# Kernel tuning notes

Hardware: AMD Instinct MI355X
Metric: run time of the kernel (lower is better)

## Reference

```python
import jax, jax.numpy as jnp
import numpy as np

D = 384; QK = 48; E = 768; LOCAL = E - D
NB = 8; NTOK = 100; NEG = -1e30
B = 128; S = 100; NPTS = 256


def layernorm(x, w, eps=1e-5):
    mu = jnp.mean(x, axis=-1, keepdims=True)
    var = jnp.mean((x - mu) ** 2, axis=-1, keepdims=True)
    return (x - mu) * jax.lax.rsqrt(var + eps) * w


def attend(q, k, v, bias=None):
    scale = 1.0 / jnp.sqrt(jnp.asarray(q.shape[-1], q.dtype))
    s = jnp.einsum('bqd,bkd->bqk', q, k) * scale
    if bias is not None:
        s = s + bias
    return jnp.einsum('bqk,bkd->bqd', jax.nn.softmax(s, axis=-1), v)


def setup_inputs() -> dict:
    key = jax.random.key(0)
    ks = jax.random.split(key, 16)
    s_exp = 0.5 / (D ** 0.5) / 2.0   # 0.5 / sqrt(residual_depth) / expand_factor
    s_prj = 1.0 / (D ** 0.5) / 2.0 / NB
    return {
        'q': jax.random.randint(ks[0], (B, S), 0, NTOK),
        'pts': jax.random.randint(ks[1], (B, NPTS, 2), 0, NTOK),
        'emb': jax.random.normal(ks[2], (NTOK, D), jnp.float32),
        'pt_emb': jax.random.normal(ks[3], (NTOK, D // 2), jnp.float32),
        'norm_w': jnp.ones((D,), jnp.float32),
        'out_w': jax.random.normal(ks[4], (NTOK, D), jnp.float32) / (D ** 0.5),
        'ln1': jnp.ones((NB, D), jnp.float32),
        'expand': s_exp * jax.random.normal(ks[5], (NB, 2 * QK + 2 * E, D), jnp.float32),
        'project1': s_prj * jax.random.normal(ks[6], (NB, D, E), jnp.float32),
        'bias_mult': jnp.ones((NB,), jnp.float32),
        'ln2': jnp.ones((NB, D), jnp.float32),
        'Wq': s_exp * jax.random.normal(ks[7], (NB, QK + 2 * LOCAL, D), jnp.float32),
        'Wkv': s_exp * jax.random.normal(ks[8], (NB, QK + 2 * D, D), jnp.float32),
        'project2': s_prj * jax.random.normal(ks[9], (NB, D, E), jnp.float32),
    }


def _forward(q, pts, emb, pt_emb, norm_w, out_w, ln1, expand, project1, bias_mult, ln2, Wq, Wkv, project2):
    x = emb[q]                                        # [B,S,D]
    kv = pt_emb[pts].reshape(pts.shape[0], -1, D)     # [B,NPTS,D] (pairs of 2D coords fold into D)
    x = layernorm(x, norm_w)

    pos = jnp.arange(x.shape[1])
    pbb = (pos[None, :] - pos[:, None]).astype(x.dtype)  # position bias base (j - i)
    allowed = pos[None, :] <= pos[:, None]                # causal: attend to past + self

    def step(h, p):
        w_ln1, W_e, W_p1, bm, w_ln2, W_q, W_kv, W_p2 = p
        # --- latent self-attention block ---
        bias = jnp.where(allowed, jax.nn.softplus(bm) * pbb, NEG)
        n = layernorm(h, w_ln1)
        proj = n @ W_e.T                                  # [B,S,2*QK+2*E]
        qr = proj[..., :QK]
        kr = proj[..., QK:2 * QK]
        lin = proj[..., 2 * QK:2 * QK + E]
        pre = proj[..., 2 * QK + E:]
        geglu = lin * jax.nn.gelu(pre, approximate=False)
        attn = attend(qr, kr, geglu[..., LOCAL:], bias)
        h = h + jnp.concatenate([geglu[..., :LOCAL], attn], axis=-1) @ W_p1.T
        # --- latent cross-attention block ---
        n = layernorm(h, w_ln2)
        pq = n @ W_q.T                                    # [B,S,QK+2*LOCAL]
        qr2 = pq[..., :QK]
        g_local = pq[..., QK:QK + LOCAL] * jax.nn.gelu(pq[..., QK + LOCAL:], approximate=False)
        pk = kv @ W_kv.T                                  # [B,NPTS,QK+2*D]
        k2 = pk[..., :QK]
        g_val = pk[..., QK:QK + D] * jax.nn.gelu(pk[..., QK + D:], approximate=False)
        attn2 = attend(qr2, k2, g_val)
        h = h + jnp.concatenate([g_local, attn2], axis=-1) @ W_p2.T
        return h, None

    x, _ = jax.lax.scan(step, x, (ln1, expand, project1, bias_mult, ln2, Wq, Wkv, project2))
    x = layernorm(x, norm_w)
    return x @ out_w.T                                    # [B,S,NTOK]


def reference(q, pts, emb, pt_emb, norm_w, out_w, ln1, expand, project1, bias_mult, ln2, Wq, Wkv, project2):
    return _forward(q, pts, emb, pt_emb, norm_w, out_w, ln1, expand, project1, bias_mult, ln2, Wq, Wkv, project2)
```

## Files before the change

### kernel.cpp

```cpp
#include <hip/hip_runtime.h>
#include <hip/hip_bf16.h>
#include <math.h>

#define B_    128
#define S_    100
#define D_    384
#define QK_   48
#define E_    768
#define LOCAL_ 384
#define NB_   8
#define NTOK_ 100
#define NPTS_ 256
#define M_    (B_*S_)

typedef unsigned short ushort;
typedef __attribute__((ext_vector_type(8))) short  bf16x8;
typedef __attribute__((ext_vector_type(8))) unsigned short ushort8v;
typedef __attribute__((ext_vector_type(4))) float  f32x4;

#define MFMA(a,b,c) __builtin_amdgcn_mfma_f32_16x16x32_bf16(a,b,c,0,0,0)

static __device__ __forceinline__ float gelu_f(float x) {
    float y = 1.5957691216057308f * (x + 0.044715f * x * x * x);
    float e = __expf(y);
    float t = 1.0f - 2.0f / (e + 1.0f);
    return 0.5f * x * (1.0f + t);
}
static __device__ __forceinline__ ushort f2b(float f) {
    union { float f; unsigned u; } x; x.f = f;
    unsigned r = x.u + 0x7FFFu + ((x.u >> 16) & 1u);
    return (ushort)(r >> 16);
}
static __device__ __forceinline__ float b2f(ushort u) {
    union { unsigned u; float f; } x; x.u = ((unsigned)u) << 16;
    return x.f;
}

__global__ __launch_bounds__(256)
void ln_rows(const float* __restrict__ X, const float* __restrict__ w,
             ushort* __restrict__ Y, int nrows)
{
    int row = blockIdx.x * 4 + (threadIdx.x >> 6);
    if (row >= nrows) return;
    int lane = threadIdx.x & 63;
    const float* x = X + (size_t)row * D_;
    float v[6]; float s = 0.f;
    #pragma unroll
    for (int t = 0; t < 6; ++t) { v[t] = x[lane + 64*t]; s += v[t]; }
    #pragma unroll
    for (int off = 32; off; off >>= 1) s += __shfl_xor(s, off);
    float mu = s * (1.f/(float)D_);
    float q = 0.f;
    #pragma unroll
    for (int t = 0; t < 6; ++t) { float d = v[t]-mu; q += d*d; }
    #pragma unroll
    for (int off = 32; off; off >>= 1) q += __shfl_xor(q, off);
    float rs = rsqrtf(q * (1.f/(float)D_) + 1e-5f);
    #pragma unroll
    for (int t = 0; t < 6; ++t)
        Y[(size_t)row*D_ + lane + 64*t] = f2b((v[t]-mu)*rs*w[lane + 64*t]);
}

__global__ __launch_bounds__(256)
void x_init(const int* __restrict__ qtok, const float* __restrict__ emb,
            const float* __restrict__ w, float* __restrict__ Y, int nrows)
{
    int row = blockIdx.x * 4 + (threadIdx.x >> 6);
    if (row >= nrows) return;
    int lane = threadIdx.x & 63;
    const float* x = emb + (size_t)qtok[row] * D_;
    float v[6]; float s = 0.f;
    #pragma unroll
    for (int t = 0; t < 6; ++t) { v[t] = x[lane + 64*t]; s += v[t]; }
    #pragma unroll
    for (int off = 32; off; off >>= 1) s += __shfl_xor(s, off);
    float mu = s * (1.f/(float)D_);
    float q = 0.f;
    #pragma unroll
    for (int t = 0; t < 6; ++t) { float d = v[t]-mu; q += d*d; }
    #pragma unroll
    for (int off = 32; off; off >>= 1) q += __shfl_xor(q, off);
    float rs = rsqrtf(q * (1.f/(float)D_) + 1e-5f);
    float* y = Y + (size_t)row * D_;
    #pragma unroll
    for (int t = 0; t < 6; ++t) y[lane + 64*t] = (v[t]-mu)*rs*w[lane + 64*t];
}

#define WE_SZ  (1632*384)
#define P1_SZ  (384*768)
#define WQ_SZ  (816*384)
#define P2_SZ  (384*768)
#define WTOT   (WE_SZ + P1_SZ + WQ_SZ + P2_SZ)

static __device__ __forceinline__ void wsplit(float v, ushort* wh, ushort* wl, size_t o) {
    ushort h = f2b(v);
    wh[o] = h; wl[o] = f2b(v - b2f(h));
}

__global__ __launch_bounds__(256)
void wconv_all_hi(const float* __restrict__ expand, const float* __restrict__ proj1,
                  const float* __restrict__ wq, const float* __restrict__ proj2,
                  ushort* __restrict__ wh)
{
    int i = blockIdx.x*256 + threadIdx.x;
    if (i >= WTOT) return;
    int blk = blockIdx.y;
    float v;
    if (i < WE_SZ) v = expand[(size_t)blk*WE_SZ + i];
    else if (i < WE_SZ+P1_SZ) v = proj1[(size_t)blk*P1_SZ + (i - WE_SZ)];
    else if (i < WE_SZ+P1_SZ+WQ_SZ) v = wq[(size_t)blk*WQ_SZ + (i - WE_SZ - P1_SZ)];
    else v = proj2[(size_t)blk*P2_SZ + (i - WE_SZ - P1_SZ - WQ_SZ)];
    wh[(size_t)blk*WTOT + i] = f2b(v);
}

__global__ __launch_bounds__(256)
void wconv_hi(const float* __restrict__ we, const float* __restrict__ p1,
              const float* __restrict__ wq, const float* __restrict__ p2,
              ushort* __restrict__ wh)
{
    int i = blockIdx.x*256 + threadIdx.x;
    if (i >= WTOT) return;
    float v;
    if (i < WE_SZ) v = we[i];
    else if (i < WE_SZ+P1_SZ) v = p1[i - WE_SZ];
    else if (i < WE_SZ+P1_SZ+WQ_SZ) v = wq[i - WE_SZ - P1_SZ];
    else v = p2[i - WE_SZ - P1_SZ - WQ_SZ];
    wh[i] = f2b(v);
}

__global__ __launch_bounds__(256)
void wconv1(const float* __restrict__ src, int n,
            ushort* __restrict__ wh, ushort* __restrict__ wl)
{
    int i = blockIdx.x*256 + threadIdx.x;
    if (i >= n) return;
    wsplit(src[i], wh, wl, i);
}

__global__ __launch_bounds__(256)
void pconv(const float* __restrict__ src, ushort* __restrict__ dst)
{
    int i = blockIdx.x*256 + threadIdx.x;
    if (i >= 128*192) return;
    int r = i / 192;
    dst[i] = (r < NTOK_) ? f2b(src[i]) : 0;
}

__global__ __launch_bounds__(256)
void mm_bt64(const ushort* __restrict__ A1, int lda1, int K1,
             const ushort* __restrict__ A2, int lda2,
             const ushort* __restrict__ Wgh, const ushort* __restrict__ Wgl,
             float* __restrict__ C, int ldc, int N, int K, int accum)
{
    __shared__ ushort Ah[64][72], Wh[64][72], Wl[64][72];
    int tid = threadIdx.x;
    int row0 = blockIdx.y*64, col0 = blockIdx.x*64;
    int srow = tid >> 3;
    int sseg = (tid & 7) * 8;
    int wid = tid >> 6, lane = tid & 63;
    int wr = wid >> 1, wc = wid & 1;
    int fr = lane & 15, fg = lane >> 4;
    f32x4 acc[2][2] = {};
    for (int k0 = 0; k0 < K; k0 += 64) {
        ushort8v va[2], vc[2], vd[2];
        #pragma unroll
        for (int p = 0; p < 2; ++p) {
            int r = p*32 + srow;
            int arow = row0 + r;
            int wrow = col0 + r;
            int gk = k0 + sseg;
            if (gk < K1) va[p] = *(const ushort8v*)(A1 + (size_t)arow*lda1 + gk);
            else         va[p] = *(const ushort8v*)(A2 + (size_t)arow*lda2 + (gk-K1));
            if (wrow >= N) wrow = N - 1;
            vc[p] = *(const ushort8v*)(Wgh + (size_t)wrow*K + gk);
            vd[p] = *(const ushort8v*)(Wgl + (size_t)wrow*K + gk);
        }
        __syncthreads();
        #pragma unroll
        for (int p = 0; p < 2; ++p) {
            int r = p*32 + srow;
            *(ushort8v*)&Ah[r][sseg] = va[p];
            *(ushort8v*)&Wh[r][sseg] = vc[p];
            *(ushort8v*)&Wl[r][sseg] = vd[p];
        }
        __syncthreads();
        #pragma unroll
        for (int kk = 0; kk < 64; kk += 32) {
            bf16x8 a[2], b_h[2], b_l[2];
            #pragma unroll
            for (int s = 0; s < 2; ++s) {
                a[s]   = *(const bf16x8*)&Ah[wr*32 + s*16 + fr][kk + fg*8];
                b_h[s] = *(const bf16x8*)&Wh[wc*32 + s*16 + fr][kk + fg*8];
                b_l[s] = *(const bf16x8*)&Wl[wc*32 + s*16 + fr][kk + fg*8];
            }
            #pragma unroll
            for (int s = 0; s < 2; ++s)
                #pragma unroll
                for (int u = 0; u < 2; ++u)
                    acc[s][u] = MFMA(a[s], b_h[u], acc[s][u]);
            #pragma unroll
            for (int s = 0; s < 2; ++s)
                #pragma unroll
                for (int u = 0; u < 2; ++u)
                    acc[s][u] = MFMA(a[s], b_l[u], acc[s][u]);
        }
        __syncthreads();
    }
    #pragma unroll
    for (int s = 0; s < 2; ++s) {
        int r = row0 + wr*32 + s*16 + fg*4;
        #pragma unroll
        for (int u = 0; u < 2; ++u) {
            int c = col0 + wc*32 + u*16 + fr;
            if (c < N) {
                #pragma unroll
                for (int j = 0; j < 4; ++j) {
                    size_t o = (size_t)(r+j)*ldc + c;
                    C[o] = accum ? (C[o] + acc[s][u][j]) : acc[s][u][j];
                }
            }
        }
    }
}

__global__ __launch_bounds__(256)
void mm_bt2(const ushort* __restrict__ A1, int lda1, int K1,
            const ushort* __restrict__ A2, int lda2,
            const ushort* __restrict__ Wgh,
            float* __restrict__ C, int ldc, int N, int K, int accum)
{
    __shared__ ushort As[128*32], Whs[64*32];
    int tid = threadIdx.x;
    int lane = tid & 63, wid = tid >> 6;
    int row0 = blockIdx.y*128, col0 = blockIdx.x*64;
    int wr = wid >> 1, wc = wid & 1;
    int fr = lane & 15, fg = lane >> 4;
    int gsl = (fg ^ ((fr >> 1) & 3)) * 8;
    int sr = tid >> 2, sg0 = tid & 3;
    int g = sg0 ^ ((sr >> 1) & 3);
    int wrow = col0 + sr; if (wrow >= N) wrow = N - 1;

    ushort8v va[2], vh;
    auto loadk = [&](int k0) {
        const ushort* Asrc; int lda, kk;
        if (k0 < K1) { Asrc = A1; lda = lda1; kk = k0; }
        else         { Asrc = A2; lda = lda2; kk = k0 - K1; }
        #pragma unroll
        for (int i = 0; i < 2; ++i)
            va[i] = *(const ushort8v*)(Asrc + (size_t)(row0 + sr + i*64)*lda + kk + g*8);
        vh = *(const ushort8v*)(Wgh + (size_t)wrow*K + k0 + g*8);
    };

    f32x4 acc[4][2] = {};
    loadk(0);
    for (int k0 = 0; k0 < K; k0 += 32) {
        __syncthreads();
        #pragma unroll
        for (int i = 0; i < 2; ++i)
            *(ushort8v*)&As[(sr + i*64)*32 + sg0*8] = va[i];
        *(ushort8v*)&Whs[sr*32 + sg0*8] = vh;
        if (k0 + 32 < K) loadk(k0 + 32);
        __syncthreads();
        bf16x8 a[4], bh[2];
        #pragma unroll
        for (int s = 0; s < 4; ++s) {
            int r = wr*64 + s*16 + fr;
            a[s] = *(const bf16x8*)&As[r*32 + gsl];
        }
        #pragma unroll
        for (int u = 0; u < 2; ++u) {
            int r = wc*32 + u*16 + fr;
            bh[u] = *(const bf16x8*)&Whs[r*32 + gsl];
        }
        #pragma unroll
        for (int s = 0; s < 4; ++s)
            #pragma unroll
            for (int u = 0; u < 2; ++u)
                acc[s][u] = MFMA(a[s], bh[u], acc[s][u]);
    }
    #pragma unroll
    for (int s = 0; s < 4; ++s) {
        int rb = row0 + wr*64 + s*16 + fg*4;
        #pragma unroll
        for (int u = 0; u < 2; ++u) {
            int c = col0 + wc*32 + u*16 + fr;
            if (c < N) {
                #pragma unroll
                for (int j = 0; j < 4; ++j) {
                    size_t o = (size_t)(rb+j)*ldc + c;
                    C[o] = accum ? (C[o] + acc[s][u][j]) : acc[s][u][j];
                }
            }
        }
    }
}

__global__ __launch_bounds__(256)
void mm_fused2(const ushort* __restrict__ Ag, int lda,
               const ushort* __restrict__ Wqh,
               int Nq, int nqt, float* __restrict__ Qout, int ldq,
               const ushort* __restrict__ W1h, const ushort* __restrict__ W2h,
               ushort* __restrict__ Oh, int ldo, int K)
{
    __shared__ ushort As[128*32];
    __shared__ ushort Xs[2][64*32];
    int tid = threadIdx.x;
    int lane = tid & 63, wid = tid >> 6;
    int row0 = blockIdx.y*128;
    int wr = wid >> 1, wc = wid & 1;
    int fr = lane & 15, fg = lane >> 4;
    int gsl = (fg ^ ((fr >> 1) & 3)) * 8;
    int sr = tid >> 2, sg0 = tid & 3;
    int g = sg0 ^ ((sr >> 1) & 3);

    if ((int)blockIdx.x < nqt) {
        int col0 = blockIdx.x*64;
        int wrow = col0 + sr; if (wrow >= Nq) wrow = Nq - 1;
        ushort8v va[2], vh;
        auto loadk = [&](int k0) {
            #pragma unroll
            for (int i = 0; i < 2; ++i)
                va[i] = *(const ushort8v*)(Ag + (size_t)(row0 + sr + i*64)*lda + k0 + g*8);
            vh = *(const ushort8v*)(Wqh + (size_t)wrow*K + k0 + g*8);
        };
        f32x4 acc[4][2] = {};
        loadk(0);
        for (int k0 = 0; k0 < K; k0 += 32) {
            __syncthreads();
            #pragma unroll
            for (int i = 0; i < 2; ++i)
                *(ushort8v*)&As[(sr + i*64)*32 + sg0*8] = va[i];
            *(ushort8v*)&Xs[0][sr*32 + sg0*8] = vh;
            if (k0 + 32 < K) loadk(k0 + 32);
            __syncthreads();
            bf16x8 a[4], bh[2];
            #pragma unroll
            for (int s = 0; s < 4; ++s) {
                int r = wr*64 + s*16 + fr;
                a[s] = *(const bf16x8*)&As[r*32 + gsl];
            }
            #pragma unroll
            for (int u = 0; u < 2; ++u) {
                int r = wc*32 + u*16 + fr;
                bh[u] = *(const bf16x8*)&Xs[0][r*32 + gsl];
            }
            #pragma unroll
            for (int s = 0; s < 4; ++s)
                #pragma unroll
                for (int u = 0; u < 2; ++u)
                    acc[s][u] = MFMA(a[s], bh[u], acc[s][u]);
        }
        #pragma unroll
        for (int s = 0; s < 4; ++s) {
            int rb = row0 + wr*64 + s*16 + fg*4;
            #pragma unroll
            for (int u = 0; u < 2; ++u) {
                int c = col0 + wc*32 + u*16 + fr;
                if (c < Nq) {
                    #pragma unroll
                    for (int j = 0; j < 4; ++j)
                        Qout[(size_t)(rb+j)*ldq + c] = acc[s][u][j];
                }
            }
        }
    } else {
        int col0 = ((int)blockIdx.x - nqt)*64;
        ushort8v va[2], vw0, vw2;
        auto loadk = [&](int k0) {
            #pragma unroll
            for (int i = 0; i < 2; ++i)
                va[i] = *(const ushort8v*)(Ag + (size_t)(row0 + sr + i*64)*lda + k0 + g*8);
            size_t wro = (size_t)(col0 + sr)*K + k0 + g*8;
            vw0 = *(const ushort8v*)(W1h + wro);
            vw2 = *(const ushort8v*)(W2h + wro);
        };
        f32x4 acc1[4][2] = {}, acc2[4][2] = {};
        loadk(0);
        for (int k0 = 0; k0 < K; k0 += 32) {
            __syncthreads();
            #pragma unroll
            for (int i = 0; i < 2; ++i)
                *(ushort8v*)&As[(sr + i*64)*32 + sg0*8] = va[i];
            {
                int o = sr*32 + sg0*8;
                *(ushort8v*)&Xs[0][o] = vw0;
                *(ushort8v*)&Xs[1][o] = vw2;
            }
            if (k0 + 32 < K) loadk(k0 + 32);
            __syncthreads();
            bf16x8 a[4], b1[2], b2[2];
            #pragma unroll
            for (int s = 0; s < 4; ++s) {
                int r = wr*64 + s*16 + fr;
                a[s] = *(const bf16x8*)&As[r*32 + gsl];
            }
            #pragma unroll
            for (int u = 0; u < 2; ++u) {
                int r = wc*32 + u*16 + fr;
                b1[u] = *(const bf16x8*)&Xs[0][r*32 + gsl];
                b2[u] = *(const bf16x8*)&Xs[1][r*32 + gsl];
            }
            #pragma unroll
            for (int s = 0; s < 4; ++s)
                #pragma unroll
                for (int u = 0; u < 2; ++u) {
                    acc1[s][u] = MFMA(a[s], b1[u], acc1[s][u]);
                    acc2[s][u] = MFMA(a[s], b2[u], acc2[s][u]);
                }
        }
        #pragma unroll
        for (int s = 0; s < 4; ++s) {
            int rb = row0 + wr*64 + s*16 + fg*4;
            #pragma unroll
            for (int u = 0; u < 2; ++u) {
                int c = col0 + wc*32 + u*16 + fr;
                #pragma unroll
                for (int j = 0; j < 4; ++j) {
                    float gg = acc1[s][u][j] * gelu_f(acc2[s][u][j]);
                    Oh[(size_t)(rb+j)*ldo + c] = f2b(gg);
                }
            }
        }
    }
}

__global__ __launch_bounds__(256)
void pk_mm(const ushort* __restrict__ A,
           const ushort* __restrict__ Wh_, const ushort* __restrict__ Wl_,
           float* __restrict__ P12)
{
    __shared__ ushort Ah[64][72], Wh[64][72], Wl[64][72];
    int tid = threadIdx.x;
    int z = blockIdx.z, blk = z >> 1, half = z & 1;
    int row0 = blockIdx.y*64, col0 = blockIdx.x*64;
    int srow = tid >> 3, sseg = (tid & 7) * 8;
    int wid = tid >> 6, lane = tid & 63;
    int wr = wid >> 1, wc = wid & 1;
    int fr = lane & 15, fg = lane >> 4;
    const ushort* Wbh = Wh_ + (size_t)blk*816*384 + half*192;
    const ushort* Wbl = Wl_ + (size_t)blk*816*384 + half*192;
    float* C = P12 + (size_t)z*128*816;
    f32x4 acc[2][2] = {};
    for (int k0 = 0; k0 < 192; k0 += 64) {
        ushort8v va[2], vc[2], vd[2];
        #pragma unroll
        for (int p = 0; p < 2; ++p) {
            int r = p*32 + srow;
            int wrow = col0 + r; if (wrow >= 816) wrow = 815;
            int gk = k0 + sseg;
            va[p] = *(const ushort8v*)(A + (size_t)(row0 + r)*192 + gk);
            vc[p] = *(const ushort8v*)(Wbh + (size_t)wrow*384 + gk);
            vd[p] = *(const ushort8v*)(Wbl + (size_t)wrow*384 + gk);
        }
        __syncthreads();
        #pragma unroll
        for (int p = 0; p < 2; ++p) {
            int r = p*32 + srow;
            *(ushort8v*)&Ah[r][sseg] = va[p];
            *(ushort8v*)&Wh[r][sseg] = vc[p];
            *(ushort8v*)&Wl[r][sseg] = vd[p];
        }
        __syncthreads();
        #pragma unroll
        for (int kk = 0; kk < 64; kk += 32) {
            bf16x8 a[2], b_h[2], b_l[2];
            #pragma unroll
            for (int s = 0; s < 2; ++s) {
                a[s]   = *(const bf16x8*)&Ah[wr*32 + s*16 + fr][kk + fg*8];
                b_h[s] = *(const bf16x8*)&Wh[wc*32 + s*16 + fr][kk + fg*8];
                b_l[s] = *(const bf16x8*)&Wl[wc*32 + s*16 + fr][kk + fg*8];
            }
            #pragma unroll
            for (int s = 0; s < 2; ++s)
                #pragma unroll
                for (int u = 0; u < 2; ++u)
                    acc[s][u] = MFMA(a[s], b_h[u], acc[s][u]);
            #pragma unroll
            for (int s = 0; s < 2; ++s)
                #pragma unroll
                for (int u = 0; u < 2; ++u)
                    acc[s][u] = MFMA(a[s], b_l[u], acc[s][u]);
        }
        __syncthreads();
    }
    #pragma unroll
    for (int s = 0; s < 2; ++s) {
        int r = row0 + wr*32 + s*16 + fg*4;
        #pragma unroll
        for (int u = 0; u < 2; ++u) {
            int c = col0 + wc*32 + u*16 + fr;
            if (c < 816) {
                #pragma unroll
                for (int j = 0; j < 4; ++j)
                    C[(size_t)(r+j)*816 + c] = acc[s][u][j];
            }
        }
    }
}

__global__ __launch_bounds__(256)
void pv2(const ushort* __restrict__ P, int ldp, long sP,
         const ushort* __restrict__ V, int ldv, long sV,
         ushort* __restrict__ Oh, int ldo, long sO,
         int Mrows, int K, int Kv)
{
    __shared__ ushort Ps[64][40];
    __shared__ ushort Vs[128*32];
    const ushort* Pb = P + (size_t)blockIdx.z * sP;
    const ushort* Vb = V + (size_t)blockIdx.z * sV;
    ushort* Ohb = Oh + (size_t)blockIdx.z * sO;
    int tid = threadIdx.x;
    int row0 = blockIdx.y*64, col0 = blockIdx.x*128;
    int wid = tid >> 6, lane = tid & 63;
    int fr = lane & 15, fg = lane >> 4;
    int prow = tid >> 2, pseg = (tid & 3) * 8;
    int vk = tid & 31, vcb = (tid >> 5) * 8;

    ushort8v pv_, vv[2];
    auto loadk = [&](int k0) {
        pv_ = (ushort8v){0,0,0,0,0,0,0,0};
        int grow = row0 + prow;
        if (grow < Mrows)
            pv_ = *(const ushort8v*)(Pb + (size_t)grow*ldp + k0 + pseg);
        vv[0] = (ushort8v){0,0,0,0,0,0,0,0};
        vv[1] = (ushort8v){0,0,0,0,0,0,0,0};
        int gk = k0 + vk;
        if (gk < Kv) {
            #pragma unroll
            for (int i = 0; i < 2; ++i)
                vv[i] = *(const ushort8v*)(Vb + (size_t)gk*ldv + col0 + vcb + i*64);
        }
    };

    f32x4 acc[4][2] = {};
    loadk(0);
    for (int k0 = 0; k0 < K; k0 += 32) {
        __syncthreads();
        *(ushort8v*)&Ps[prow][pseg] = pv_;
        #pragma unroll
        for (int i = 0; i < 2; ++i) {
            #pragma unroll
            for (int e = 0; e < 8; ++e) {
                int c = vcb + i*64 + e;
                Vs[c*32 + (vk & 7) + 8*((vk >> 3) ^ ((c >> 3) & 3))] = vv[i][e];
            }
        }
        if (k0 + 32 < K) loadk(k0 + 32);
        __syncthreads();
        bf16x8 a[4], b[2];
        #pragma unroll
        for (int s = 0; s < 4; ++s)
            a[s] = *(const bf16x8*)&Ps[s*16 + fr][fg*8];
        #pragma unroll
        for (int u = 0; u < 2; ++u) {
            int c = wid*32 + u*16 + fr;
            b[u] = *(const bf16x8*)&Vs[c*32 + 8*(fg ^ ((c >> 3) & 3))];
        }
        #pragma unroll
        for (int s = 0; s < 4; ++s)
            #pragma unroll
            for (int u = 0; u < 2; ++u)
                acc[s][u] = MFMA(a[s], b[u], acc[s][u]);
    }
    #pragma unroll
    for (int s = 0; s < 4; ++s) {
        int rbase = row0 + s*16 + fg*4;
        #pragma unroll
        for (int u = 0; u < 2; ++u) {
            int c = col0 + wid*32 + u*16 + fr;
            #pragma unroll
            for (int j = 0; j < 4; ++j) {
                int r = rbase + j;
                if (r < Mrows)
                    Ohb[(size_t)r*ldo + c] = f2b(acc[s][u][j]);
            }
        }
    }
}

__global__ __launch_bounds__(256)
void attn1_score(const float* __restrict__ qk, const float* __restrict__ bm, int blk,
                 ushort* __restrict__ P)
{
    __shared__ float qrs[50][QK_];
    __shared__ float krs[S_][QK_+1];
    int b = blockIdx.x, r0 = blockIdx.y*50;
    int tid = threadIdx.x;
    for (int idx = tid; idx < 50*QK_; idx += 256) {
        int r = idx / QK_, c = idx % QK_;
        qrs[r][c] = qk[((size_t)(b*S_ + r0 + r))*96 + c];
    }
    for (int idx = tid; idx < S_*QK_; idx += 256) {
        int r = idx / QK_, c = idx % QK_;
        krs[r][c] = qk[((size_t)(b*S_ + r))*96 + 48 + c];
    }
    __syncthreads();
    float bmv = bm[blk];
    float sp = (bmv > 20.f) ? bmv : log1pf(expf(bmv));
    const float scale = 0.14433756729740643f;
    int w = tid >> 6, lane = tid & 63;
    for (int t = 0; t < 13; ++t) {
        int li = w + 4*t;
        if (li >= 50) break;
        int i = r0 + li;
        int j1 = lane, j2 = lane + 64;
        float s1 = -1e30f, s2 = -1e30f;
        if (j1 <= i) {
            float acc = 0.f;
            #pragma unroll
            for (int l = 0; l < QK_; ++l) acc += qrs[li][l]*krs[j1][l];
            s1 = acc*scale + sp*(float)(j1 - i);
        }
        if (j2 <= i) {
            float acc = 0.f;
            #pragma unroll
            for (int l = 0; l < QK_; ++l) acc += qrs[li][l]*krs[j2][l];
            s2 = acc*scale + sp*(float)(j2 - i);
        }
        float m = fmaxf(s1, s2);
        #pragma unroll
        for (int off = 32; off; off >>= 1) m = fmaxf(m, __shfl_xor(m, off));
        float p1 = (j1 <= i) ? expf(s1 - m) : 0.f;
        float p2 = (j2 <= i) ? expf(s2 - m) : 0.f;
        float sum = p1 + p2;
        #pragma unroll
        for (int off = 32; off; off >>= 1) sum += __shfl_xor(sum, off);
        float inv = 1.f / sum;
        ushort* prow = P + ((size_t)(b*S_) + i)*128;
        prow[j1] = f2b(p1*inv);
        prow[j2] = f2b(p2*inv);
    }
}

__global__ __launch_bounds__(256)
void attn2_score(const float* __restrict__ q2, const float* __restrict__ k2,
                 ushort* __restrict__ P)
{
    __shared__ float ks[NPTS_][QK_+1];
    int b = blockIdx.x, r0 = blockIdx.y*20;
    int tid = threadIdx.x;
    for (int idx = tid; idx < NPTS_*QK_; idx += 256) {
        int r = idx / QK_, c = idx % QK_;
        ks[r][c] = k2[((size_t)(b*NPTS_ + r))*QK_ + c];
    }
    __syncthreads();
    const float scale = 0.14433756729740643f;
    int w = tid >> 6, lane = tid & 63;
    for (int t = 0; t < 5; ++t) {
        int i = r0 + w + 4*t;
        const float* qr = q2 + ((size_t)(b*S_ + i))*QK_;
        float s[4] = {0.f,0.f,0.f,0.f};
        for (int l = 0; l < QK_; ++l) {
            float ql = qr[l];
            #pragma unroll
            for (int r = 0; r < 4; ++r) s[r] += ql * ks[lane + 64*r][l];
        }
        #pragma unroll
        for (int r = 0; r < 4; ++r) s[r] *= scale;
        float m = fmaxf(fmaxf(s[0],s[1]), fmaxf(s[2],s[3]));
        #pragma unroll
        for (int off = 32; off; off >>= 1) m = fmaxf(m, __shfl_xor(m, off));
        float p[4]; float sum = 0.f;
        #pragma unroll
        for (int r = 0; r < 4; ++r) { p[r] = expf(s[r]-m); sum += p[r]; }
        #pragma unroll
        for (int off = 32; off; off >>= 1) sum += __shfl_xor(sum, off);
        float inv = 1.f / sum;
        ushort* prow = P + ((size_t)(b*S_) + i)*256;
        #pragma unroll
        for (int r = 0; r < 4; ++r) prow[lane + 64*r] = f2b(p[r]*inv);
    }
}

__global__ __launch_bounds__(256)
void pk_gather(const int* __restrict__ pts, const float* __restrict__ P12, int blk,
               float* __restrict__ k2, ushort* __restrict__ gv)
{
    int pair = blockIdx.x*4 + (threadIdx.x >> 6);
    int lane = threadIdx.x & 63;
    const float* P1 = P12 + (size_t)(blk*2 + 0)*128*816;
    const float* P2 = P12 + (size_t)(blk*2 + 1)*128*816;
    int t0 = pts[2*pair], t1 = pts[2*pair+1];
    const float* a = P1 + (size_t)t0*816;
    const float* c = P2 + (size_t)t1*816;
    if (lane < QK_) k2[(size_t)pair*QK_ + lane] = a[lane] + c[lane];
    #pragma unroll
    for (int t = 0; t < 6; ++t) {
        int i = lane + 64*t;
        float lin = a[48 + i] + c[48 + i];
        float pre = a[432 + i] + c[432 + i];
        gv[(size_t)pair*D_ + i] = f2b(lin * gelu_f(pre));
    }
}

extern "C" void kernel_launch(void* const* d_in, const int* in_sizes, int n_in,
                              void* d_out, int out_size, void* d_ws, size_t ws_size,
                              hipStream_t stream)
{
    const int*   qtok  = (const int*)d_in[0];
    const int*   pts   = (const int*)d_in[1];
    const float* emb   = (const float*)d_in[2];
    const float* ptemb = (const float*)d_in[3];
    const float* normw = (const float*)d_in[4];
    const float* outw  = (const float*)d_in[5];
    const float* ln1   = (const float*)d_in[6];
    const float* expand= (const float*)d_in[7];
    const float* proj1 = (const float*)d_in[8];
    const float* bm    = (const float*)d_in[9];
    const float* ln2   = (const float*)d_in[10];
    const float* Wq    = (const float*)d_in[11];
    const float* Wkv   = (const float*)d_in[12];
    const float* proj2 = (const float*)d_in[13];
    float* out = (float*)d_out;

    char* base = (char*)d_ws;
    size_t off = 0;
    auto alloc = [&](size_t bytes){ void* p = base + off; off += (bytes + 255) & ~(size_t)255; return p; };
    float*  h     = (float*) alloc((size_t)M_*D_*4);
    ushort* nh    = (ushort*)alloc((size_t)M_*D_*2);
    float*  qk1   = (float*) alloc((size_t)M_*96*4);
    ushort* gegl  = (ushort*)alloc((size_t)M_*E_*2);
    ushort* atb   = (ushort*)alloc((size_t)M_*D_*2);
    ushort* Pbuf  = (ushort*)alloc((size_t)M_*256*2);
    ushort* gv    = (ushort*)alloc((size_t)B_*NPTS_*D_*2);
    float*  P12   = (float*) alloc((size_t)16*128*816*4);
    float*  k2    = (float*) alloc((size_t)B_*NPTS_*QK_*4);
    ushort* wkvh  = (ushort*)alloc((size_t)NB_*816*384*2);
    ushort* wkvl  = (ushort*)alloc((size_t)NB_*816*384*2);
    ushort* ptp   = (ushort*)alloc((size_t)128*192*2);
    ushort* obh   = (ushort*)alloc((size_t)NTOK_*D_*2);
    ushort* obl   = (ushort*)alloc((size_t)NTOK_*D_*2);

    size_t rem = (ws_size > off) ? (ws_size - off) : 0;
    bool fits8 = rem >= ((size_t)NB_ * WTOT * 2 + 1024);
    int nlay = fits8 ? NB_ : 1;
    ushort* wbh = (ushort*)alloc((size_t)nlay*WTOT*2);
    size_t wstride = fits8 ? (size_t)WTOT : 0;

    float*  qr2   = qk1;
    ushort* gloc  = gegl;

    const size_t oWE = 0;
    const size_t oP1 = WE_SZ;
    const size_t oWQ = WE_SZ + P1_SZ;
    const size_t oP2 = WE_SZ + P1_SZ + WQ_SZ;

    x_init<<<M_/4, 256, 0, stream>>>(qtok, emb, normw, h, M_);
    pconv<<<(128*192 + 255)/256, 256, 0, stream>>>(ptemb, ptp);
    wconv1<<<(NB_*816*384 + 255)/256, 256, 0, stream>>>(Wkv, NB_*816*384, wkvh, wkvl);
    pk_mm<<<dim3(13, 2, 16), 256, 0, stream>>>(ptp, wkvh, wkvl, P12);
    if (fits8)
        wconv_all_hi<<<dim3((WTOT+255)/256, NB_), 256, 0, stream>>>(
            expand, proj1, Wq, proj2, wbh);

    for (int blk = 0; blk < NB_; ++blk) {
        if (!fits8)
            wconv_hi<<<(WTOT+255)/256, 256, 0, stream>>>(
                expand + (size_t)blk*WE_SZ, proj1 + (size_t)blk*P1_SZ,
                Wq + (size_t)blk*WQ_SZ, proj2 + (size_t)blk*P2_SZ, wbh);
        const ushort* Lh = wbh + wstride*blk;

        ln_rows<<<M_/4, 256, 0, stream>>>(h, ln1 + blk*D_, nh, M_);
        mm_fused2<<<dim3(14, M_/128), 256, 0, stream>>>(nh, D_,
            Lh + oWE, 96, 2, qk1, 96,
            Lh + oWE + (size_t)96*D_, Lh + oWE + (size_t)864*D_,
            gegl, E_, D_);
        attn1_score<<<dim3(B_,2), 256, 0, stream>>>(qk1, bm, blk, Pbuf);
        pv2<<<dim3(3,2,B_), 256, 0, stream>>>(Pbuf, 128, (long)S_*128,
            gegl + LOCAL_, E_, (long)S_*E_,
            atb, D_, (long)S_*D_, S_, 128, S_);
        mm_bt2<<<dim3(6, M_/128), 256, 0, stream>>>(gegl, E_, D_, atb, D_,
            Lh + oP1, h, D_, D_, E_, 1);

        ln_rows<<<M_/4, 256, 0, stream>>>(h, ln2 + blk*D_, nh, M_);
        mm_fused2<<<dim3(7, M_/128), 256, 0, stream>>>(nh, D_,
            Lh + oWQ, 48, 1, qr2, 48,
            Lh + oWQ + (size_t)48*D_, Lh + oWQ + (size_t)432*D_,
            gloc, D_, D_);
        pk_gather<<<B_*NPTS_/4, 256, 0, stream>>>(pts, P12, blk, k2, gv);
        attn2_score<<<dim3(B_,5), 256, 0, stream>>>(qr2, k2, Pbuf);
        pv2<<<dim3(3,2,B_), 256, 0, stream>>>(Pbuf, 256, (long)S_*256,
            gv, D_, (long)NPTS_*D_,
            atb, D_, (long)S_*D_, S_, 256, 256);
        mm_bt2<<<dim3(6, M_/128), 256, 0, stream>>>(gloc, D_, D_, atb, D_,
            Lh + oP2, h, D_, D_, E_, 1);
    }

    ln_rows<<<M_/4, 256, 0, stream>>>(h, normw, nh, M_);
    wconv1<<<(NTOK_*D_ + 255)/256, 256, 0, stream>>>(outw, NTOK_*D_, obh, obl);
    mm_bt64<<<dim3(2, M_/64), 256, 0, stream>>>(nh, D_, D_, nh, D_,
        obh, obl, out, NTOK_, NTOK_, D_, 0);
}
```

Before: 1.809 ms.

## Double-buffer LDS tiles in GEMM and PV kernels to drop a barrier per step

Converts the mm_bt2, mm_fused2 and pv2 K-loops to ping-pong shared-memory buffers. The next tile is stored into the alternate buffer after the MFMAs, so each iteration needs one __syncthreads instead of two. The goal is less barrier stall and better overlap of global loads with compute. In exchange LDS use per block doubles, which may reduce occupancy.

```diff
diff --git a/kernel.cpp b/kernel.cpp
--- a/kernel.cpp
+++ b/kernel.cpp
@@ -229,7 +229,7 @@
             const ushort* __restrict__ Wgh,
             float* __restrict__ C, int ldc, int N, int K, int accum)
 {
-    __shared__ ushort As[128*32], Whs[64*32];
+    __shared__ ushort As[2][128*32], Whs[2][64*32];
     int tid = threadIdx.x;
     int lane = tid & 63, wid = tid >> 6;
     int row0 = blockIdx.y*128, col0 = blockIdx.x*64;
@@ -250,33 +250,39 @@
             va[i] = *(const ushort8v*)(Asrc + (size_t)(row0 + sr + i*64)*lda + kk + g*8);
         vh = *(const ushort8v*)(Wgh + (size_t)wrow*K + k0 + g*8);
     };
-
+    auto store = [&](int buf) {
+        #pragma unroll
+        for (int i = 0; i < 2; ++i)
+            *(ushort8v*)&As[buf][(sr + i*64)*32 + sg0*8] = va[i];
+        *(ushort8v*)&Whs[buf][sr*32 + sg0*8] = vh;
+    };
+
+    int nsteps = K >> 5;
     f32x4 acc[4][2] = {};
     loadk(0);
-    for (int k0 = 0; k0 < K; k0 += 32) {
-        __syncthreads();
-        #pragma unroll
-        for (int i = 0; i < 2; ++i)
-            *(ushort8v*)&As[(sr + i*64)*32 + sg0*8] = va[i];
-        *(ushort8v*)&Whs[sr*32 + sg0*8] = vh;
-        if (k0 + 32 < K) loadk(k0 + 32);
-        __syncthreads();
+    store(0);
+    __syncthreads();
+    for (int t = 0; t < nsteps; ++t) {
+        int buf = t & 1;
+        if (t + 1 < nsteps) loadk((t+1)*32);
         bf16x8 a[4], bh[2];
         #pragma unroll
         for (int s = 0; s < 4; ++s) {
             int r = wr*64 + s*16 + fr;
-            a[s] = *(const bf16x8*)&As[r*32 + gsl];
+            a[s] = *(const bf16x8*)&As[buf][r*32 + gsl];
         }
         #pragma unroll
         for (int u = 0; u < 2; ++u) {
             int r = wc*32 + u*16 + fr;
-            bh[u] = *(const bf16x8*)&Whs[r*32 + gsl];
+            bh[u] = *(const bf16x8*)&Whs[buf][r*32 + gsl];
         }
         #pragma unroll
         for (int s = 0; s < 4; ++s)
             #pragma unroll
             for (int u = 0; u < 2; ++u)
                 acc[s][u] = MFMA(a[s], bh[u], acc[s][u]);
+        if (t + 1 < nsteps) store(buf ^ 1);
+        __syncthreads();
     }
     #pragma unroll
     for (int s = 0; s < 4; ++s) {
@@ -302,8 +308,8 @@
                const ushort* __restrict__ W1h, const ushort* __restrict__ W2h,
                ushort* __restrict__ Oh, int ldo, int K)
 {
-    __shared__ ushort As[128*32];
-    __shared__ ushort Xs[2][64*32];
+    __shared__ ushort As[2][128*32];
+    __shared__ ushort Xs[2][2][64*32];
     int tid = threadIdx.x;
     int lane = tid & 63, wid = tid >> 6;
     int row0 = blockIdx.y*128;
@@ -312,6 +318,7 @@
     int gsl = (fg ^ ((fr >> 1) & 3)) * 8;
     int sr = tid >> 2, sg0 = tid & 3;
     int g = sg0 ^ ((sr >> 1) & 3);
+    int nsteps = K >> 5;
 
     if ((int)blockIdx.x < nqt) {
         int col0 = blockIdx.x*64;
@@ -323,32 +330,37 @@
                 va[i] = *(const ushort8v*)(Ag + (size_t)(row0 + sr + i*64)*lda + k0 + g*8);
             vh = *(const ushort8v*)(Wqh + (size_t)wrow*K + k0 + g*8);
         };
+        auto store = [&](int buf) {
+            #pragma unroll
+            for (int i = 0; i < 2; ++i)
+                *(ushort8v*)&As[buf][(sr + i*64)*32 + sg0*8] = va[i];
+            *(ushort8v*)&Xs[buf][0][sr*32 + sg0*8] = vh;
+        };
         f32x4 acc[4][2] = {};
         loadk(0);
-        for (int k0 = 0; k0 < K; k0 += 32) {
-            __syncthreads();
-            #pragma unroll
-            for (int i = 0; i < 2; ++i)
-                *(ushort8v*)&As[(sr + i*64)*32 + sg0*8] = va[i];
-            *(ushort8v*)&Xs[0][sr*32 + sg0*8] = vh;
-            if (k0 + 32 < K) loadk(k0 + 32);
-            __syncthreads();
+        store(0);
+        __syncthreads();
+        for (int t = 0; t < nsteps; ++t) {
+            int buf = t & 1;
+            if (t + 1 < nsteps) loadk((t+1)*32);
             bf16x8 a[4], bh[2];
             #pragma unroll
             for (int s = 0; s < 4; ++s) {
                 int r = wr*64 + s*16 + fr;
-                a[s] = *(const bf16x8*)&As[r*32 + gsl];
+                a[s] = *(const bf16x8*)&As[buf][r*32 + gsl];
             }
             #pragma unroll
             for (int u = 0; u < 2; ++u) {
                 int r = wc*32 + u*16 + fr;
-                bh[u] = *(const bf16x8*)&Xs[0][r*32 + gsl];
+                bh[u] = *(const bf16x8*)&Xs[buf][0][r*32 + gsl];
             }
             #pragma unroll
             for (int s = 0; s < 4; ++s)
                 #pragma unroll
                 for (int u = 0; u < 2; ++u)
                     acc[s][u] = MFMA(a[s], bh[u], acc[s][u]);
+            if (t + 1 < nsteps) store(buf ^ 1);
+            __syncthreads();
         }
         #pragma unroll
         for (int s = 0; s < 4; ++s) {
@@ -374,31 +386,32 @@
             vw0 = *(const ushort8v*)(W1h + wro);
             vw2 = *(const ushort8v*)(W2h + wro);
         };
+        auto store = [&](int buf) {
+            #pragma unroll
+            for (int i = 0; i < 2; ++i)
+                *(ushort8v*)&As[buf][(sr + i*64)*32 + sg0*8] = va[i];
+            int o = sr*32 + sg0*8;
+            *(ushort8v*)&Xs[buf][0][o] = vw0;
+            *(ushort8v*)&Xs[buf][1][o] = vw2;
+        };
         f32x4 acc1[4][2] = {}, acc2[4][2] = {};
         loadk(0);
-        for (int k0 = 0; k0 < K; k0 += 32) {
-            __syncthreads();
-            #pragma unroll
-            for (int i = 0; i < 2; ++i)
-                *(ushort8v*)&As[(sr + i*64)*32 + sg0*8] = va[i];
-            {
-                int o = sr*32 + sg0*8;
-                *(ushort8v*)&Xs[0][o] = vw0;
-                *(ushort8v*)&Xs[1][o] = vw2;
-            }
-            if (k0 + 32 < K) loadk(k0 + 32);
-            __syncthreads();
+        store(0);
+        __syncthreads();
+        for (int t = 0; t < nsteps; ++t) {
+            int buf = t & 1;
+            if (t + 1 < nsteps) loadk((t+1)*32);
             bf16x8 a[4], b1[2], b2[2];
             #pragma unroll
             for (int s = 0; s < 4; ++s) {
                 int r = wr*64 + s*16 + fr;
-                a[s] = *(const bf16x8*)&As[r*32 + gsl];
+                a[s] = *(const bf16x8*)&As[buf][r*32 + gsl];
             }
             #pragma unroll
             for (int u = 0; u < 2; ++u) {
                 int r = wc*32 + u*16 + fr;
-                b1[u] = *(const bf16x8*)&Xs[0][r*32 + gsl];
-                b2[u] = *(const bf16x8*)&Xs[1][r*32 + gsl];
+                b1[u] = *(const bf16x8*)&Xs[buf][0][r*32 + gsl];
+                b2[u] = *(const bf16x8*)&Xs[buf][1][r*32 + gsl];
             }
             #pragma unroll
             for (int s = 0; s < 4; ++s)
@@ -407,6 +420,8 @@
                     acc1[s][u] = MFMA(a[s], b1[u], acc1[s][u]);
                     acc2[s][u] = MFMA(a[s], b2[u], acc2[s][u]);
                 }
+            if (t + 1 < nsteps) store(buf ^ 1);
+            __syncthreads();
         }
         #pragma unroll
         for (int s = 0; s < 4; ++s) {
@@ -504,8 +519,8 @@
          ushort* __restrict__ Oh, int ldo, long sO,
          int Mrows, int K, int Kv)
 {
-    __shared__ ushort Ps[64][40];
-    __shared__ ushort Vs[128*32];
+    __shared__ ushort Ps[2][64*40];
+    __shared__ ushort Vs[2][128*32];
     const ushort* Pb = P + (size_t)blockIdx.z * sP;
     const ushort* Vb = V + (size_t)blockIdx.z * sV;
     ushort* Ohb = Oh + (size_t)blockIdx.z * sO;
@@ -531,36 +546,42 @@
                 vv[i] = *(const ushort8v*)(Vb + (size_t)gk*ldv + col0 + vcb + i*64);
         }
     };
-
+    auto store = [&](int buf) {
+        *(ushort8v*)&Ps[buf][prow*40 + pseg] = pv_;
+        #pragma unroll
+        for (int i = 0; i < 2; ++i) {
+            #pragma unroll
+            for (int e = 0; e < 8; ++e) {
+                int c = vcb + i*64 + e;
+                Vs[buf][c*32 + (vk & 7) + 8*((vk >> 3) ^ ((c >> 3) & 3))] = vv[i][e];
+            }
+        }
+    };
+
+    int nsteps = K >> 5;
     f32x4 acc[4][2] = {};
     loadk(0);
-    for (int k0 = 0; k0 < K; k0 += 32) {
-        __syncthreads();
-        *(ushort8v*)&Ps[prow][pseg] = pv_;
-        #pragma unroll
-        for (int i = 0; i < 2; ++i) {
-            #pragma unroll
-            for (int e = 0; e < 8; ++e) {
-                int c = vcb + i*64 + e;
-                Vs[c*32 + (vk & 7) + 8*((vk >> 3) ^ ((c >> 3) & 3))] = vv[i][e];
-            }
-        }
-        if (k0 + 32 < K) loadk(k0 + 32);
-        __syncthreads();
+    store(0);
+    __syncthreads();
+    for (int t = 0; t < nsteps; ++t) {
+        int buf = t & 1;
+        if (t + 1 < nsteps) loadk((t+1)*32);
         bf16x8 a[4], b[2];
         #pragma unroll
         for (int s = 0; s < 4; ++s)
-            a[s] = *(const bf16x8*)&Ps[s*16 + fr][fg*8];
+            a[s] = *(const bf16x8*)&Ps[buf][(s*16 + fr)*40 + fg*8];
         #pragma unroll
         for (int u = 0; u < 2; ++u) {
             int c = wid*32 + u*16 + fr;
-            b[u] = *(const bf16x8*)&Vs[c*32 + 8*(fg ^ ((c >> 3) & 3))];
+            b[u] = *(const bf16x8*)&Vs[buf][c*32 + 8*(fg ^ ((c >> 3) & 3))];
         }
         #pragma unroll
         for (int s = 0; s < 4; ++s)
             #pragma unroll
             for (int u = 0; u < 2; ++u)
                 acc[s][u] = MFMA(a[s], b[u], acc[s][u]);
+        if (t + 1 < nsteps) store(buf ^ 1);
+        __syncthreads();
     }
     #pragma unroll
     for (int s = 0; s < 4; ++s) {
```

Measured after the change: 1.814 ms. No clear change (+0.3%).
